# Kernel tuning notes

Measured on AMD Instinct MI355X. Metric: run time of the kernel, lower is better.

The kernel has to match this reference:

```python
import jax, jax.numpy as jnp
import numpy as np

NBITS = 4
GROUP_SIZE = 128


def setup_inputs() -> dict:
    key = jax.random.key(0)
    k1, k2, k3, k4, k5 = jax.random.split(key, 5)
    B, S, K, N = 2, 2048, 4096, 4096
    G = K // GROUP_SIZE  # 32 groups along K
    x = jax.random.normal(k1, (B, S, K), dtype=jnp.float16)
    # unpacked uint4 weights stored in int32 carrier, values in [0, 2^nbits)
    W_q = jax.random.randint(k2, (N, K), 0, 2 ** NBITS, dtype=jnp.int32)
    scale = (jax.random.uniform(k3, (N, G), dtype=jnp.float32) * 0.01 + 0.001).astype(jnp.float16)
    zero = (jax.random.uniform(k4, (N, G), dtype=jnp.float32) * (2 ** NBITS)).astype(jnp.float16)
    bias = jax.random.normal(k5, (N,), dtype=jnp.float16)
    return {"x": x, "W_q": W_q, "scale": scale, "zero": zero, "bias": bias}


def _dequant(W_q, scale, zero):
    # W_q: [N, K] int, scale/zero: [N, K//group_size] fp16
    # zeros_mode='original': W = (W_q - zero) * scale, per group along K
    N, K = W_q.shape
    G = K // GROUP_SIZE
    Wg = W_q.reshape(N, G, GROUP_SIZE).astype(jnp.float16)
    Wd = (Wg - zero[:, :, None]) * scale[:, :, None]
    return Wd.reshape(N, K)


def reference(x, W_q, scale, zero, bias):
    # out = x @ W_deq^T + bias   (layout 'nt': W is [N, K])
    W = _dequant(W_q, scale, zero)            # [N, K] fp16
    out = jnp.einsum('bsk,nk->bsn', x, W)     # [B, S, N] fp16 accum per module config
    return out + bias
```

## Files before the change

kernel.cpp:

```cpp
#include <hip/hip_runtime.h>
#include <hip/hip_bf16.h>


typedef __bf16 bf16x8 __attribute__((ext_vector_type(8)));
typedef float f32x4 __attribute__((ext_vector_type(4)));

#define BM 128
#define BN 128
#define BK 64

static __device__ __forceinline__ int pack_bf16x2(float a, float b) {
    __hip_bfloat162 p = __float22bfloat162_rn(make_float2(a, b));
    int r;
    __builtin_memcpy(&r, &p, 4);
    return r;
}

__global__ __launch_bounds__(256) void prepass_kernel(
    const float* __restrict__ X, unsigned short* __restrict__ Ad,
    const int*   __restrict__ Wq,
    const float* __restrict__ scale,
    const float* __restrict__ zero,
    unsigned short* __restrict__ Wd,
    int aUnits, int wUnits, int K, int G, int GROUP)
{
    const int stride = gridDim.x * blockDim.x;
    const int t0     = blockIdx.x * blockDim.x + threadIdx.x;

    for (int u = t0; u < aUnits; u += stride) {
        const long long f = (long long)u * 8;
        const float4 a0 = *(const float4*)(X + f);
        const float4 a1 = *(const float4*)(X + f + 4);
        int4 d;
        d.x = pack_bf16x2(a0.x, a0.y);
        d.y = pack_bf16x2(a0.z, a0.w);
        d.z = pack_bf16x2(a1.x, a1.y);
        d.w = pack_bf16x2(a1.z, a1.w);
        *(int4*)(Ad + f) = d;
    }

    const int unitsPerRow = K >> 3;
    for (int u = t0; u < wUnits; u += stride) {
        const int n = u / unitsPerRow;
        const int k = (u - n * unitsPerRow) * 8;
        const int g = k / GROUP;
        const float s  = scale[(long long)n * G + g];
        const float z  = zero [(long long)n * G + g];
        const float mz = -z * s;

        const long long f = (long long)n * K + k;
        const int4 q0 = *(const int4*)(Wq + f);
        const int4 q1 = *(const int4*)(Wq + f + 4);
        int4 d;
        d.x = pack_bf16x2((float)q0.x * s + mz, (float)q0.y * s + mz);
        d.y = pack_bf16x2((float)q0.z * s + mz, (float)q0.w * s + mz);
        d.z = pack_bf16x2((float)q1.x * s + mz, (float)q1.y * s + mz);
        d.w = pack_bf16x2((float)q1.z * s + mz, (float)q1.w * s + mz);
        *(int4*)(Wd + f) = d;
    }
}

__global__ __launch_bounds__(512, 2) void gemm256_8ph(
    const unsigned short* __restrict__ A,
    const unsigned short* __restrict__ Bw,
    const float* __restrict__ bias,
    float*       __restrict__ C,
    int M, int N, int K)
{
    __shared__ unsigned short ldsA[2][2][8192];
    __shared__ unsigned short ldsB[2][2][8192];

    const int tid  = threadIdx.x;
    const int lane = tid & 63;
    const int wave = tid >> 6;
    const int wm   = wave >> 2;
    const int wn   = wave & 3;

    const int nwg  = (N >> 8) * (M >> 8);
    const int cpx  = nwg >> 3;
    const int bid  = blockIdx.x;
    const int wgid = (bid & 7) * cpx + (bid >> 3);
    const int bx   = wgid % (N >> 8);
    const int by   = wgid / (N >> 8);
    const int blockN0 = bx << 8;
    const int blockM0 = by << 8;

    long long gSrcA[2], gSrcB[2];
    int ldsDst[2];
#pragma unroll
    for (int l = 0; l < 2; ++l) {
        const int s  = l * 512 + tid;
        const int R  = s >> 3;
        const int j  = s & 7;
        const int ju = j ^ (R & 7);
        const int r  = 2 * R + (ju >> 2);
        const int cc = ju & 3;
        gSrcA[l] = (long long)(blockM0 + r) * K + cc * 8;
        gSrcB[l] = (long long)(blockN0 + r) * K + cc * 8;
        ldsDst[l] = (l * 512 + wave * 64) * 8;
    }

    const int row16 = lane & 15;
    const int quad  = lane >> 4;
    int offA[8], offB[4];
#pragma unroll
    for (int m = 0; m < 8; ++m) {
        const int r = wm * 128 + m * 16 + row16;
        const int R = r >> 1;
        const int j = (((r & 1) << 2) | quad) ^ (R & 7);
        offA[m] = R * 64 + j * 8;
    }
#pragma unroll
    for (int n = 0; n < 4; ++n) {
        const int r = wn * 64 + n * 16 + row16;
        const int R = r >> 1;
        const int j = (((r & 1) << 2) | quad) ^ (R & 7);
        offB[n] = R * 64 + j * 8;
    }

    f32x4 acc[8][4];
#pragma unroll
    for (int m = 0; m < 8; ++m)
#pragma unroll
        for (int n = 0; n < 4; ++n)
            acc[m][n] = (f32x4){0.f, 0.f, 0.f, 0.f};

#define STAGE_A(T_, KH_)                                                      \
    do {                                                                      \
        const int b_ = (T_) & 1;                                              \
        const long long ko_ = (long long)(T_) * 64 + (KH_) * 32;              \
        __builtin_amdgcn_global_load_lds(                                     \
            (const __attribute__((address_space(1))) unsigned int*)           \
                (A + gSrcA[0] + ko_),                                         \
            (__attribute__((address_space(3))) unsigned int*)                 \
                (&ldsA[b_][KH_][ldsDst[0]]), 16, 0, 0);                       \
        __builtin_amdgcn_global_load_lds(                                     \
            (const __attribute__((address_space(1))) unsigned int*)           \
                (A + gSrcA[1] + ko_),                                         \
            (__attribute__((address_space(3))) unsigned int*)                 \
                (&ldsA[b_][KH_][ldsDst[1]]), 16, 0, 0);                       \
    } while (0)

#define STAGE_B(T_, KH_)                                                      \
    do {                                                                      \
        const int b_ = (T_) & 1;                                              \
        const long long ko_ = (long long)(T_) * 64 + (KH_) * 32;              \
        __builtin_amdgcn_global_load_lds(                                     \
            (const __attribute__((address_space(1))) unsigned int*)           \
                (Bw + gSrcB[0] + ko_),                                        \
            (__attribute__((address_space(3))) unsigned int*)                 \
                (&ldsB[b_][KH_][ldsDst[0]]), 16, 0, 0);                       \
        __builtin_amdgcn_global_load_lds(                                     \
            (const __attribute__((address_space(1))) unsigned int*)           \
                (Bw + gSrcB[1] + ko_),                                        \
            (__attribute__((address_space(3))) unsigned int*)                 \
                (&ldsB[b_][KH_][ldsDst[1]]), 16, 0, 0);                       \
    } while (0)

#define READ_BV(c_, kk_)                                                      \
    bv0 = *(const bf16x8*)&ldsB[c_][kk_][offB[0]];                            \
    bv1 = *(const bf16x8*)&ldsB[c_][kk_][offB[1]];                            \
    bv2 = *(const bf16x8*)&ldsB[c_][kk_][offB[2]];                            \
    bv3 = *(const bf16x8*)&ldsB[c_][kk_][offB[3]];

#define READ_AV(c_, kk_, mh_)                                                 \
    av0 = *(const bf16x8*)&ldsA[c_][kk_][offA[(mh_) * 4 + 0]];                \
    av1 = *(const bf16x8*)&ldsA[c_][kk_][offA[(mh_) * 4 + 1]];                \
    av2 = *(const bf16x8*)&ldsA[c_][kk_][offA[(mh_) * 4 + 2]];                \
    av3 = *(const bf16x8*)&ldsA[c_][kk_][offA[(mh_) * 4 + 3]];

#define MFROW(mi_, av_)                                                       \
    acc[mi_][0] = __builtin_amdgcn_mfma_f32_16x16x32_bf16(av_, bv0, acc[mi_][0], 0, 0, 0); \
    acc[mi_][1] = __builtin_amdgcn_mfma_f32_16x16x32_bf16(av_, bv1, acc[mi_][1], 0, 0, 0); \
    acc[mi_][2] = __builtin_amdgcn_mfma_f32_16x16x32_bf16(av_, bv2, acc[mi_][2], 0, 0, 0); \
    acc[mi_][3] = __builtin_amdgcn_mfma_f32_16x16x32_bf16(av_, bv3, acc[mi_][3], 0, 0, 0);

#define MFMA16(mh_)                                                           \
    __builtin_amdgcn_s_setprio(1);                                            \
    MFROW((mh_) * 4 + 0, av0);                                                \
    MFROW((mh_) * 4 + 1, av1);                                                \
    MFROW((mh_) * 4 + 2, av2);                                                \
    MFROW((mh_) * 4 + 3, av3);                                                \
    __builtin_amdgcn_s_setprio(0);

    const int NT = K >> 6;

    STAGE_A(0, 0); STAGE_B(0, 0); STAGE_A(0, 1); STAGE_B(0, 1);
    STAGE_A(1, 0); STAGE_B(1, 0); STAGE_A(1, 1);
    asm volatile("s_waitcnt vmcnt(6)" ::: "memory");
    __builtin_amdgcn_s_barrier();

    bf16x8 av0, av1, av2, av3, bv0, bv1, bv2, bv3;

#pragma unroll 2
    for (int T = 0; T <= NT - 3; ++T) {
        const int c = T & 1;
        READ_BV(c, 0);
        READ_AV(c, 0, 0);
        STAGE_B(T + 1, 1);
        __builtin_amdgcn_s_barrier();
        MFMA16(0);
        READ_AV(c, 0, 1);
        STAGE_A(T + 2, 0);
        __builtin_amdgcn_s_barrier();
        MFMA16(1);
        READ_BV(c, 1);
        READ_AV(c, 1, 0);
        STAGE_B(T + 2, 0);
        __builtin_amdgcn_s_barrier();
        MFMA16(0);
        READ_AV(c, 1, 1);
        STAGE_A(T + 2, 1);
        asm volatile("s_waitcnt vmcnt(6)" ::: "memory");
        __builtin_amdgcn_s_barrier();
        MFMA16(1);
    }

    STAGE_B(NT - 1, 1);
    asm volatile("s_waitcnt vmcnt(0)" ::: "memory");
    __builtin_amdgcn_s_barrier();
    {
        const int c = (NT - 2) & 1;
        READ_BV(c, 0); READ_AV(c, 0, 0); MFMA16(0);
        READ_AV(c, 0, 1); MFMA16(1);
        READ_BV(c, 1); READ_AV(c, 1, 0); MFMA16(0);
        READ_AV(c, 1, 1); MFMA16(1);
    }
    {
        const int c = (NT - 1) & 1;
        READ_BV(c, 0); READ_AV(c, 0, 0); MFMA16(0);
        READ_AV(c, 0, 1); MFMA16(1);
        READ_BV(c, 1); READ_AV(c, 1, 0); MFMA16(0);
        READ_AV(c, 1, 1); MFMA16(1);
    }

#undef STAGE_A
#undef STAGE_B
#undef READ_BV
#undef READ_AV
#undef MFROW
#undef MFMA16

    const int colBase = blockN0 + wn * 64;
    const int rowBase = blockM0 + wm * 128;
    float biasf[4];
#pragma unroll
    for (int n = 0; n < 4; ++n)
        biasf[n] = bias[colBase + n * 16 + row16];

#pragma unroll
    for (int m = 0; m < 8; ++m) {
        const int row0 = rowBase + m * 16 + quad * 4;
#pragma unroll
        for (int n = 0; n < 4; ++n) {
            const int col = colBase + n * 16 + row16;
#pragma unroll
            for (int r = 0; r < 4; ++r) {
                C[(long long)(row0 + r) * N + col] = acc[m][n][r] + biasf[n];
            }
        }
    }
}

__global__ __launch_bounds__(256, 2) void gemm_bf16_nt(
    const unsigned short* __restrict__ A,
    const unsigned short* __restrict__ Bw,
    const float* __restrict__ bias,
    float*       __restrict__ C,
    int M, int N, int K)
{
    __shared__ unsigned short ldsA[BM * BK];
    __shared__ unsigned short ldsB[BN * BK];

    const int tid   = threadIdx.x;
    const int lane  = tid & 63;
    const int wave  = tid >> 6;
    const int waveM = wave >> 1;
    const int waveN = wave & 1;

    const int blockN0 = blockIdx.x * BN;
    const int blockM0 = blockIdx.y * BM;

    const long long aBase = (long long)blockM0 * K;
    const long long bBase = (long long)blockN0 * K;

    const int rowInChunk = lane >> 3;
    const int colChunkSw = (lane & 7) ^ rowInChunk;
    const int col8       = colChunkSw * 8;

    f32x4 acc[4][4];
#pragma unroll
    for (int i = 0; i < 4; ++i)
#pragma unroll
        for (int j = 0; j < 4; ++j)
            acc[i][j] = (f32x4){0.f, 0.f, 0.f, 0.f};

    const int row16 = lane & 15;
    const int quad  = lane >> 4;
    const int sw    = row16 & 7;

    for (int k0 = 0; k0 < K; k0 += BK) {
        __syncthreads();
#pragma unroll
        for (int c = 0; c < 4; ++c) {
            const int chunk = (wave << 2) | c;
            const int row   = (chunk << 3) | rowInChunk;
            const unsigned short* gA = A  + aBase + (long long)row * K + k0 + col8;
            const unsigned short* gB = Bw + bBase + (long long)row * K + k0 + col8;
            __builtin_amdgcn_global_load_lds(
                (const __attribute__((address_space(1))) unsigned int*)gA,
                (__attribute__((address_space(3))) unsigned int*)&ldsA[chunk * 512],
                16, 0, 0);
            __builtin_amdgcn_global_load_lds(
                (const __attribute__((address_space(1))) unsigned int*)gB,
                (__attribute__((address_space(3))) unsigned int*)&ldsB[chunk * 512],
                16, 0, 0);
        }
        __syncthreads();

#pragma unroll
        for (int kk = 0; kk < 2; ++kk) {
            bf16x8 av[4], bv[4];
#pragma unroll
            for (int i = 0; i < 4; ++i) {
                const int r    = waveM * 64 + i * 16 + row16;
                const int slot = (kk * 4 + quad) ^ sw;
                av[i] = *(const bf16x8*)&ldsA[r * BK + slot * 8];
            }
#pragma unroll
            for (int j = 0; j < 4; ++j) {
                const int r    = waveN * 64 + j * 16 + row16;
                const int slot = (kk * 4 + quad) ^ sw;
                bv[j] = *(const bf16x8*)&ldsB[r * BK + slot * 8];
            }
#pragma unroll
            for (int i = 0; i < 4; ++i)
#pragma unroll
                for (int j = 0; j < 4; ++j)
                    acc[i][j] = __builtin_amdgcn_mfma_f32_16x16x32_bf16(
                        av[i], bv[j], acc[i][j], 0, 0, 0);
        }
    }

    const int colBase = blockN0 + waveN * 64;
    const int rowBase = blockM0 + waveM * 64;
    float biasf[4];
#pragma unroll
    for (int j = 0; j < 4; ++j)
        biasf[j] = bias[colBase + j * 16 + row16];

#pragma unroll
    for (int i = 0; i < 4; ++i) {
        const int row0 = rowBase + i * 16 + quad * 4;
#pragma unroll
        for (int j = 0; j < 4; ++j) {
            const int col = colBase + j * 16 + row16;
#pragma unroll
            for (int r = 0; r < 4; ++r) {
                C[(long long)(row0 + r) * N + col] = acc[i][j][r] + biasf[j];
            }
        }
    }
}

__global__ __launch_bounds__(256) void hqq_gemm_fused_f32(
    const float* __restrict__ A,
    const int*   __restrict__ Wq,
    const float* __restrict__ scale,
    const float* __restrict__ zero,
    const float* __restrict__ bias,
    float*       __restrict__ C,
    int M, int N, int K, int G, int GROUP)
{
    __shared__ unsigned short ldsA[BM * BK];
    __shared__ unsigned short ldsB[BN * BK];

    const int tid   = threadIdx.x;
    const int lane  = tid & 63;
    const int wave  = tid >> 6;
    const int waveM = wave >> 1;
    const int waveN = wave & 1;

    const int blockN0 = blockIdx.x * BN;
    const int blockM0 = blockIdx.y * BM;

    const int row16 = lane & 15;
    const int quad  = lane >> 4;

    f32x4 acc[4][4];
#pragma unroll
    for (int i = 0; i < 4; ++i)
#pragma unroll
        for (int j = 0; j < 4; ++j)
            acc[i][j] = (f32x4){0.f, 0.f, 0.f, 0.f};

    for (int k0 = 0; k0 < K; k0 += BK) {
        const int g = k0 / GROUP;
        int4 ra[4], rb[4];
#pragma unroll
        for (int c = 0; c < 4; ++c) {
            const int chunk = c * 256 + tid;
            const int row   = chunk >> 3;
            const int col   = (chunk & 7) * 8;

            const float* ap = A + (long long)(blockM0 + row) * K + k0 + col;
            const float4 a0 = *(const float4*)(ap);
            const float4 a1 = *(const float4*)(ap + 4);
            int4 da;
            da.x = pack_bf16x2(a0.x, a0.y);
            da.y = pack_bf16x2(a0.z, a0.w);
            da.z = pack_bf16x2(a1.x, a1.y);
            da.w = pack_bf16x2(a1.z, a1.w);
            ra[c] = da;

            const int n = blockN0 + row;
            const float s  = scale[(long long)n * G + g];
            const float z  = zero [(long long)n * G + g];
            const float mz = -z * s;
            const long long wb = (long long)n * K + k0 + col;
            const int4 q0 = *(const int4*)(Wq + wb);
            const int4 q1 = *(const int4*)(Wq + wb + 4);
            int4 db;
            db.x = pack_bf16x2((float)q0.x * s + mz, (float)q0.y * s + mz);
            db.y = pack_bf16x2((float)q0.z * s + mz, (float)q0.w * s + mz);
            db.z = pack_bf16x2((float)q1.x * s + mz, (float)q1.y * s + mz);
            db.w = pack_bf16x2((float)q1.z * s + mz, (float)q1.w * s + mz);
            rb[c] = db;
        }

        __syncthreads();
#pragma unroll
        for (int c = 0; c < 4; ++c) {
            const int chunk = c * 256 + tid;
            *(int4*)&ldsA[chunk * 8] = ra[c];
            *(int4*)&ldsB[chunk * 8] = rb[c];
        }
        __syncthreads();

#pragma unroll
        for (int kk = 0; kk < 2; ++kk) {
            const int kOff = kk * 32 + quad * 8;
            bf16x8 av[4], bv[4];
#pragma unroll
            for (int i = 0; i < 4; ++i)
                av[i] = *(const bf16x8*)&ldsA[(waveM * 64 + i * 16 + row16) * BK + kOff];
#pragma unroll
            for (int j = 0; j < 4; ++j)
                bv[j] = *(const bf16x8*)&ldsB[(waveN * 64 + j * 16 + row16) * BK + kOff];
#pragma unroll
            for (int i = 0; i < 4; ++i)
#pragma unroll
                for (int j = 0; j < 4; ++j)
                    acc[i][j] = __builtin_amdgcn_mfma_f32_16x16x32_bf16(
                        av[i], bv[j], acc[i][j], 0, 0, 0);
        }
    }

    const int colBase = blockN0 + waveN * 64;
    const int rowBase = blockM0 + waveM * 64;
    float biasf[4];
#pragma unroll
    for (int j = 0; j < 4; ++j)
        biasf[j] = bias[colBase + j * 16 + row16];

#pragma unroll
    for (int i = 0; i < 4; ++i) {
        const int row0 = rowBase + i * 16 + quad * 4;
#pragma unroll
        for (int j = 0; j < 4; ++j) {
            const int col = colBase + j * 16 + row16;
#pragma unroll
            for (int r = 0; r < 4; ++r) {
                C[(long long)(row0 + r) * N + col] = acc[i][j][r] + biasf[j];
            }
        }
    }
}

extern "C" void kernel_launch(void* const* d_in, const int* in_sizes, int n_in,
                              void* d_out, int out_size, void* d_ws, size_t ws_size,
                              hipStream_t stream) {
    (void)n_in; (void)out_size;

    const float* x     = (const float*)d_in[0];
    const int*   Wq    = (const int*)d_in[1];
    const float* scale = (const float*)d_in[2];
    const float* zero  = (const float*)d_in[3];
    const float* bias  = (const float*)d_in[4];
    float*       out   = (float*)d_out;

    const int N     = in_sizes[4];
    const int G     = in_sizes[2] / N;
    const int K     = in_sizes[1] / N;
    const int M     = in_sizes[0] / K;
    const int GROUP = K / G;

    const size_t needWs = (size_t)N * K * 2 + (size_t)M * K * 2;

    if (ws_size >= needWs) {
        unsigned short* Wd = (unsigned short*)d_ws;
        unsigned short* Ad = (unsigned short*)((char*)d_ws + (size_t)N * K * 2);

        const int aUnits = (int)((long long)M * K / 8);
        const int wUnits = (int)((long long)N * K / 8);
        prepass_kernel<<<2048, 256, 0, stream>>>(x, Ad, Wq, scale, zero, Wd,
                                                 aUnits, wUnits, K, G, GROUP);

        const int nwg = (N >> 8) * (M >> 8);
        const int NT  = K >> 6;
        if ((M % 256) == 0 && (N % 256) == 0 && (K % 64) == 0 && NT >= 4 &&
            (nwg % 8) == 0) {
            gemm256_8ph<<<nwg, 512, 0, stream>>>(Ad, Wd, bias, out, M, N, K);
        } else {
            dim3 grid(N / BN, M / BM);
            gemm_bf16_nt<<<grid, 256, 0, stream>>>(Ad, Wd, bias, out, M, N, K);
        }
    } else {
        dim3 grid(N / BN, M / BM);
        hqq_gemm_fused_f32<<<grid, 256, 0, stream>>>(x, Wq, scale, zero, bias, out,
                                                     M, N, K, G, GROUP);
    }
}
```

Before: 283.9 us.

## Fuse dequant and bf16 conversion into pipelined 256x256 GEMM, drop prepass

Removes the separate prepass that converted x to bf16 and dequantized W into workspace. The 256x256 GEMM now loads fp32 activations and int32 weights into registers, converts and dequantizes them, and writes bf16 into LDS inside a restructured software pipeline with explicit vmcnt waits. This avoids writing and re-reading the bf16 copies through memory. In exchange each tile moves twice as many global bytes (fp32/int32 instead of bf16), uses more VGPRs, and gives up the direct global-to-LDS load path.

```diff
diff --git a/kernel.cpp b/kernel.cpp
--- a/kernel.cpp
+++ b/kernel.cpp
@@ -4,10 +4,6 @@
 
 typedef __bf16 bf16x8 __attribute__((ext_vector_type(8)));
 typedef float f32x4 __attribute__((ext_vector_type(4)));
-
-#define BM 128
-#define BN 128
-#define BK 64
 
 static __device__ __forceinline__ int pack_bf16x2(float a, float b) {
     __hip_bfloat162 p = __float22bfloat162_rn(make_float2(a, b));
@@ -16,56 +12,17 @@
     return r;
 }
 
-__global__ __launch_bounds__(256) void prepass_kernel(
-    const float* __restrict__ X, unsigned short* __restrict__ Ad,
+struct ARegs { float4 v[2][2]; };
+struct BRegs { int4   q[2][2]; };
+
+__global__ __launch_bounds__(512, 2) void hqq_gemm256_fused(
+    const float* __restrict__ X,
     const int*   __restrict__ Wq,
     const float* __restrict__ scale,
     const float* __restrict__ zero,
-    unsigned short* __restrict__ Wd,
-    int aUnits, int wUnits, int K, int G, int GROUP)
-{
-    const int stride = gridDim.x * blockDim.x;
-    const int t0     = blockIdx.x * blockDim.x + threadIdx.x;
-
-    for (int u = t0; u < aUnits; u += stride) {
-        const long long f = (long long)u * 8;
-        const float4 a0 = *(const float4*)(X + f);
-        const float4 a1 = *(const float4*)(X + f + 4);
-        int4 d;
-        d.x = pack_bf16x2(a0.x, a0.y);
-        d.y = pack_bf16x2(a0.z, a0.w);
-        d.z = pack_bf16x2(a1.x, a1.y);
-        d.w = pack_bf16x2(a1.z, a1.w);
-        *(int4*)(Ad + f) = d;
-    }
-
-    const int unitsPerRow = K >> 3;
-    for (int u = t0; u < wUnits; u += stride) {
-        const int n = u / unitsPerRow;
-        const int k = (u - n * unitsPerRow) * 8;
-        const int g = k / GROUP;
-        const float s  = scale[(long long)n * G + g];
-        const float z  = zero [(long long)n * G + g];
-        const float mz = -z * s;
-
-        const long long f = (long long)n * K + k;
-        const int4 q0 = *(const int4*)(Wq + f);
-        const int4 q1 = *(const int4*)(Wq + f + 4);
-        int4 d;
-        d.x = pack_bf16x2((float)q0.x * s + mz, (float)q0.y * s + mz);
-        d.y = pack_bf16x2((float)q0.z * s + mz, (float)q0.w * s + mz);
-        d.z = pack_bf16x2((float)q1.x * s + mz, (float)q1.y * s + mz);
-        d.w = pack_bf16x2((float)q1.z * s + mz, (float)q1.w * s + mz);
-        *(int4*)(Wd + f) = d;
-    }
-}
-
-__global__ __launch_bounds__(512, 2) void gemm256_8ph(
-    const unsigned short* __restrict__ A,
-    const unsigned short* __restrict__ Bw,
     const float* __restrict__ bias,
     float*       __restrict__ C,
-    int M, int N, int K)
+    int M, int N, int K, int G)
 {
     __shared__ unsigned short ldsA[2][2][8192];
     __shared__ unsigned short ldsB[2][2][8192];
@@ -86,7 +43,7 @@
     const int blockM0 = by << 8;
 
     long long gSrcA[2], gSrcB[2];
-    int ldsDst[2];
+    int nIdx[2], wrElem[2];
 #pragma unroll
     for (int l = 0; l < 2; ++l) {
         const int s  = l * 512 + tid;
@@ -95,9 +52,10 @@
         const int ju = j ^ (R & 7);
         const int r  = 2 * R + (ju >> 2);
         const int cc = ju & 3;
-        gSrcA[l] = (long long)(blockM0 + r) * K + cc * 8;
-        gSrcB[l] = (long long)(blockN0 + r) * K + cc * 8;
-        ldsDst[l] = (l * 512 + wave * 64) * 8;
+        gSrcA[l]  = (long long)(blockM0 + r) * K + cc * 8;
+        gSrcB[l]  = (long long)(blockN0 + r) * K + cc * 8;
+        nIdx[l]   = blockN0 + r;
+        wrElem[l] = s * 8;
     }
 
     const int row16 = lane & 15;
@@ -125,36 +83,63 @@
         for (int n = 0; n < 4; ++n)
             acc[m][n] = (f32x4){0.f, 0.f, 0.f, 0.f};
 
-#define STAGE_A(T_, KH_)                                                      \
+#define LOAD_A(dst_, T_, KH_)                                                 \
     do {                                                                      \
-        const int b_ = (T_) & 1;                                              \
         const long long ko_ = (long long)(T_) * 64 + (KH_) * 32;              \
-        __builtin_amdgcn_global_load_lds(                                     \
-            (const __attribute__((address_space(1))) unsigned int*)           \
-                (A + gSrcA[0] + ko_),                                         \
-            (__attribute__((address_space(3))) unsigned int*)                 \
-                (&ldsA[b_][KH_][ldsDst[0]]), 16, 0, 0);                       \
-        __builtin_amdgcn_global_load_lds(                                     \
-            (const __attribute__((address_space(1))) unsigned int*)           \
-                (A + gSrcA[1] + ko_),                                         \
-            (__attribute__((address_space(3))) unsigned int*)                 \
-                (&ldsA[b_][KH_][ldsDst[1]]), 16, 0, 0);                       \
+        _Pragma("unroll")                                                     \
+        for (int l = 0; l < 2; ++l) {                                         \
+            const float* p_ = X + gSrcA[l] + ko_;                             \
+            dst_.v[l][0] = *(const float4*)p_;                                \
+            dst_.v[l][1] = *(const float4*)(p_ + 4);                          \
+        }                                                                     \
     } while (0)
 
-#define STAGE_B(T_, KH_)                                                      \
+#define LOAD_B(dst_, T_, KH_)                                                 \
     do {                                                                      \
-        const int b_ = (T_) & 1;                                              \
         const long long ko_ = (long long)(T_) * 64 + (KH_) * 32;              \
-        __builtin_amdgcn_global_load_lds(                                     \
-            (const __attribute__((address_space(1))) unsigned int*)           \
-                (Bw + gSrcB[0] + ko_),                                        \
-            (__attribute__((address_space(3))) unsigned int*)                 \
-                (&ldsB[b_][KH_][ldsDst[0]]), 16, 0, 0);                       \
-        __builtin_amdgcn_global_load_lds(                                     \
-            (const __attribute__((address_space(1))) unsigned int*)           \
-                (Bw + gSrcB[1] + ko_),                                        \
-            (__attribute__((address_space(3))) unsigned int*)                 \
-                (&ldsB[b_][KH_][ldsDst[1]]), 16, 0, 0);                       \
+        _Pragma("unroll")                                                     \
+        for (int l = 0; l < 2; ++l) {                                         \
+            const int* p_ = Wq + gSrcB[l] + ko_;                              \
+            dst_.q[l][0] = *(const int4*)p_;                                  \
+            dst_.q[l][1] = *(const int4*)(p_ + 4);                           \
+        }                                                                     \
+    } while (0)
+
+#define WRITE_A(buf_, kh_, rgs_)                                              \
+    do {                                                                      \
+        _Pragma("unroll")                                                     \
+        for (int l = 0; l < 2; ++l) {                                         \
+            int4 d_;                                                          \
+            d_.x = pack_bf16x2(rgs_.v[l][0].x, rgs_.v[l][0].y);               \
+            d_.y = pack_bf16x2(rgs_.v[l][0].z, rgs_.v[l][0].w);               \
+            d_.z = pack_bf16x2(rgs_.v[l][1].x, rgs_.v[l][1].y);               \
+            d_.w = pack_bf16x2(rgs_.v[l][1].z, rgs_.v[l][1].w);               \
+            *(int4*)&ldsA[buf_][kh_][wrElem[l]] = d_;                         \
+        }                                                                     \
+    } while (0)
+
+#define WRITE_B(buf_, kh_, rgs_, s0_, z0_, s1_, z1_)                          \
+    do {                                                                      \
+        {                                                                     \
+            const float s_ = (s0_), mz_ = -(z0_) * (s0_);                     \
+            const int4 q0_ = rgs_.q[0][0], q1_ = rgs_.q[0][1];                \
+            int4 d_;                                                          \
+            d_.x = pack_bf16x2((float)q0_.x * s_ + mz_, (float)q0_.y * s_ + mz_); \
+            d_.y = pack_bf16x2((float)q0_.z * s_ + mz_, (float)q0_.w * s_ + mz_); \
+            d_.z = pack_bf16x2((float)q1_.x * s_ + mz_, (float)q1_.y * s_ + mz_); \
+            d_.w = pack_bf16x2((float)q1_.z * s_ + mz_, (float)q1_.w * s_ + mz_); \
+            *(int4*)&ldsB[buf_][kh_][wrElem[0]] = d_;                         \
+        }                                                                     \
+        {                                                                     \
+            const float s_ = (s1_), mz_ = -(z1_) * (s1_);                     \
+            const int4 q0_ = rgs_.q[1][0], q1_ = rgs_.q[1][1];                \
+            int4 d_;                                                          \
+            d_.x = pack_bf16x2((float)q0_.x * s_ + mz_, (float)q0_.y * s_ + mz_); \
+            d_.y = pack_bf16x2((float)q0_.z * s_ + mz_, (float)q0_.w * s_ + mz_); \
+            d_.z = pack_bf16x2((float)q1_.x * s_ + mz_, (float)q1_.y * s_ + mz_); \
+            d_.w = pack_bf16x2((float)q1_.z * s_ + mz_, (float)q1_.w * s_ + mz_); \
+            *(int4*)&ldsB[buf_][kh_][wrElem[1]] = d_;                         \
+        }                                                                     \
     } while (0)
 
 #define READ_BV(c_, kk_)                                                      \
@@ -183,63 +168,116 @@
     MFROW((mh_) * 4 + 3, av3);                                                \
     __builtin_amdgcn_s_setprio(0);
 
+#define VMW(n_)  asm volatile("s_waitcnt vmcnt(" #n_ ")" ::: "memory")
+#define LGKM0()  asm volatile("s_waitcnt lgkmcnt(0)" ::: "memory")
+#define BAR()    __builtin_amdgcn_s_barrier()
+
     const int NT = K >> 6;
 
-    STAGE_A(0, 0); STAGE_B(0, 0); STAGE_A(0, 1); STAGE_B(0, 1);
-    STAGE_A(1, 0); STAGE_B(1, 0); STAGE_A(1, 1);
-    asm volatile("s_waitcnt vmcnt(6)" ::: "memory");
-    __builtin_amdgcn_s_barrier();
+    ARegs a00, a01, a10, A_f1;
+    BRegs b00, b01, b11, B_i0;
+    float sP0, sP1, zP0, zP1;
+    sP0 = scale[(long long)nIdx[0] * G];
+    sP1 = scale[(long long)nIdx[1] * G];
+    zP0 = zero [(long long)nIdx[0] * G];
+    zP1 = zero [(long long)nIdx[1] * G];
+    LOAD_A(a00, 0, 0); LOAD_B(b00, 0, 0);
+    LOAD_A(a01, 0, 1); LOAD_B(b01, 0, 1);
+    LOAD_A(a10, 1, 0); LOAD_B(b11, 1, 1);
+    VMW(0);
+    WRITE_A(0, 0, a00); WRITE_B(0, 0, b00, sP0, zP0, sP1, zP1);
+    WRITE_A(0, 1, a01); WRITE_B(0, 1, b01, sP0, zP0, sP1, zP1);
+    WRITE_A(1, 0, a10); WRITE_B(1, 1, b11, sP0, zP0, sP1, zP1);
+    LOAD_A(A_f1, 1, 1);
+    LOAD_B(B_i0, 1, 0);
+    LGKM0(); BAR();
 
     bf16x8 av0, av1, av2, av3, bv0, bv1, bv2, bv3;
 
 #pragma unroll 2
     for (int T = 0; T <= NT - 3; ++T) {
-        const int c = T & 1;
+        const int c = T & 1, cn = c ^ 1;
+        ARegs A_f0n, A_f1n;
+        BRegs B_i1n, B_i0n;
+        float sN0, sN1, zN0, zN1;
         READ_BV(c, 0);
         READ_AV(c, 0, 0);
-        STAGE_B(T + 1, 1);
-        __builtin_amdgcn_s_barrier();
+        VMW(4);
+        WRITE_A(cn, 1, A_f1);
+        {
+            const long long g2 = (T + 2) >> 1;
+            sN0 = scale[(long long)nIdx[0] * G + g2];
+            zN0 = zero [(long long)nIdx[0] * G + g2];
+            sN1 = scale[(long long)nIdx[1] * G + g2];
+            zN1 = zero [(long long)nIdx[1] * G + g2];
+        }
+        LOAD_A(A_f0n, T + 2, 0);
+        LGKM0(); BAR();
         MFMA16(0);
         READ_AV(c, 0, 1);
-        STAGE_A(T + 2, 0);
-        __builtin_amdgcn_s_barrier();
+        VMW(8);
+        WRITE_B(cn, 0, B_i0, sP0, zP0, sP1, zP1);
+        LOAD_B(B_i1n, T + 2, 1);
+        LGKM0(); BAR();
         MFMA16(1);
         READ_BV(c, 1);
         READ_AV(c, 1, 0);
-        STAGE_B(T + 2, 0);
-        __builtin_amdgcn_s_barrier();
+        VMW(4);
+        WRITE_A(c, 0, A_f0n);
+        LOAD_A(A_f1n, T + 2, 1);
+        LGKM0(); BAR();
         MFMA16(0);
         READ_AV(c, 1, 1);
-        STAGE_A(T + 2, 1);
-        asm volatile("s_waitcnt vmcnt(6)" ::: "memory");
-        __builtin_amdgcn_s_barrier();
-        MFMA16(1);
-    }
-
-    STAGE_B(NT - 1, 1);
-    asm volatile("s_waitcnt vmcnt(0)" ::: "memory");
-    __builtin_amdgcn_s_barrier();
+        VMW(4);
+        WRITE_B(c, 1, B_i1n, sN0, zN0, sN1, zN1);
+        LOAD_B(B_i0n, T + 2, 0);
+        LGKM0(); BAR();
+        MFMA16(1);
+        A_f1 = A_f1n; B_i0 = B_i0n;
+        sP0 = sN0; sP1 = sN1; zP0 = zN0; zP1 = zN1;
+    }
+
     {
-        const int c = (NT - 2) & 1;
-        READ_BV(c, 0); READ_AV(c, 0, 0); MFMA16(0);
-        READ_AV(c, 0, 1); MFMA16(1);
-        READ_BV(c, 1); READ_AV(c, 1, 0); MFMA16(0);
-        READ_AV(c, 1, 1); MFMA16(1);
-    }
-    {
-        const int c = (NT - 1) & 1;
-        READ_BV(c, 0); READ_AV(c, 0, 0); MFMA16(0);
-        READ_AV(c, 0, 1); MFMA16(1);
-        READ_BV(c, 1); READ_AV(c, 1, 0); MFMA16(0);
-        READ_AV(c, 1, 1); MFMA16(1);
-    }
-
-#undef STAGE_A
-#undef STAGE_B
+        const int c2 = (NT - 2) & 1, c1 = (NT - 1) & 1;
+        READ_BV(c2, 0);
+        READ_AV(c2, 0, 0);
+        VMW(4);
+        WRITE_A(c1, 1, A_f1);
+        LGKM0(); BAR();
+        MFMA16(0);
+        READ_AV(c2, 0, 1);
+        VMW(0);
+        WRITE_B(c1, 0, B_i0, sP0, zP0, sP1, zP1);
+        LGKM0(); BAR();
+        MFMA16(1);
+        READ_BV(c2, 1);
+        READ_AV(c2, 1, 0);
+        MFMA16(0);
+        READ_AV(c2, 1, 1);
+        MFMA16(1);
+        READ_BV(c1, 0);
+        READ_AV(c1, 0, 0);
+        MFMA16(0);
+        READ_AV(c1, 0, 1);
+        MFMA16(1);
+        READ_BV(c1, 1);
+        READ_AV(c1, 1, 0);
+        MFMA16(0);
+        READ_AV(c1, 1, 1);
+        MFMA16(1);
+    }
+
+#undef LOAD_A
+#undef LOAD_B
+#undef WRITE_A
+#undef WRITE_B
 #undef READ_BV
 #undef READ_AV
 #undef MFROW
 #undef MFMA16
+#undef VMW
+#undef LGKM0
+#undef BAR
 
     const int colBase = blockN0 + wn * 64;
     const int rowBase = blockM0 + wm * 128;
@@ -262,106 +300,9 @@
     }
 }
 
-__global__ __launch_bounds__(256, 2) void gemm_bf16_nt(
-    const unsigned short* __restrict__ A,
-    const unsigned short* __restrict__ Bw,
-    const float* __restrict__ bias,
-    float*       __restrict__ C,
-    int M, int N, int K)
-{
-    __shared__ unsigned short ldsA[BM * BK];
-    __shared__ unsigned short ldsB[BN * BK];
-
-    const int tid   = threadIdx.x;
-    const int lane  = tid & 63;
-    const int wave  = tid >> 6;
-    const int waveM = wave >> 1;
-    const int waveN = wave & 1;
-
-    const int blockN0 = blockIdx.x * BN;
-    const int blockM0 = blockIdx.y * BM;
-
-    const long long aBase = (long long)blockM0 * K;
-    const long long bBase = (long long)blockN0 * K;
-
-    const int rowInChunk = lane >> 3;
-    const int colChunkSw = (lane & 7) ^ rowInChunk;
-    const int col8       = colChunkSw * 8;
-
-    f32x4 acc[4][4];
-#pragma unroll
-    for (int i = 0; i < 4; ++i)
-#pragma unroll
-        for (int j = 0; j < 4; ++j)
-            acc[i][j] = (f32x4){0.f, 0.f, 0.f, 0.f};
-
-    const int row16 = lane & 15;
-    const int quad  = lane >> 4;
-    const int sw    = row16 & 7;
-
-    for (int k0 = 0; k0 < K; k0 += BK) {
-        __syncthreads();
-#pragma unroll
-        for (int c = 0; c < 4; ++c) {
-            const int chunk = (wave << 2) | c;
-            const int row   = (chunk << 3) | rowInChunk;
-            const unsigned short* gA = A  + aBase + (long long)row * K + k0 + col8;
-            const unsigned short* gB = Bw + bBase + (long long)row * K + k0 + col8;
-            __builtin_amdgcn_global_load_lds(
-                (const __attribute__((address_space(1))) unsigned int*)gA,
-                (__attribute__((address_space(3))) unsigned int*)&ldsA[chunk * 512],
-                16, 0, 0);
-            __builtin_amdgcn_global_load_lds(
-                (const __attribute__((address_space(1))) unsigned int*)gB,
-                (__attribute__((address_space(3))) unsigned int*)&ldsB[chunk * 512],
-                16, 0, 0);
-        }
-        __syncthreads();
-
-#pragma unroll
-        for (int kk = 0; kk < 2; ++kk) {
-            bf16x8 av[4], bv[4];
-#pragma unroll
-            for (int i = 0; i < 4; ++i) {
-                const int r    = waveM * 64 + i * 16 + row16;
-                const int slot = (kk * 4 + quad) ^ sw;
-                av[i] = *(const bf16x8*)&ldsA[r * BK + slot * 8];
-            }
-#pragma unroll
-            for (int j = 0; j < 4; ++j) {
-                const int r    = waveN * 64 + j * 16 + row16;
-                const int slot = (kk * 4 + quad) ^ sw;
-                bv[j] = *(const bf16x8*)&ldsB[r * BK + slot * 8];
-            }
-#pragma unroll
-            for (int i = 0; i < 4; ++i)
-#pragma unroll
-                for (int j = 0; j < 4; ++j)
-                    acc[i][j] = __builtin_amdgcn_mfma_f32_16x16x32_bf16(
-                        av[i], bv[j], acc[i][j], 0, 0, 0);
-        }
-    }
-
-    const int colBase = blockN0 + waveN * 64;
-    const int rowBase = blockM0 + waveM * 64;
-    float biasf[4];
-#pragma unroll
-    for (int j = 0; j < 4; ++j)
-        biasf[j] = bias[colBase + j * 16 + row16];
-
-#pragma unroll
-    for (int i = 0; i < 4; ++i) {
-        const int row0 = rowBase + i * 16 + quad * 4;
-#pragma unroll
-        for (int j = 0; j < 4; ++j) {
-            const int col = colBase + j * 16 + row16;
-#pragma unroll
-            for (int r = 0; r < 4; ++r) {
-                C[(long long)(row0 + r) * N + col] = acc[i][j][r] + biasf[j];
-            }
-        }
-    }
-}
+#define BM 128
+#define BN 128
+#define BK 64
 
 __global__ __launch_bounds__(256) void hqq_gemm_fused_f32(
     const float* __restrict__ A,
@@ -480,7 +421,7 @@
 extern "C" void kernel_launch(void* const* d_in, const int* in_sizes, int n_in,
                               void* d_out, int out_size, void* d_ws, size_t ws_size,
                               hipStream_t stream) {
-    (void)n_in; (void)out_size;
+    (void)n_in; (void)out_size; (void)d_ws; (void)ws_size;
 
     const float* x     = (const float*)d_in[0];
     const int*   Wq    = (const int*)d_in[1];
@@ -495,26 +436,12 @@
     const int M     = in_sizes[0] / K;
     const int GROUP = K / G;
 
-    const size_t needWs = (size_t)N * K * 2 + (size_t)M * K * 2;
-
-    if (ws_size >= needWs) {
-        unsigned short* Wd = (unsigned short*)d_ws;
-        unsigned short* Ad = (unsigned short*)((char*)d_ws + (size_t)N * K * 2);
-
-        const int aUnits = (int)((long long)M * K / 8);
-        const int wUnits = (int)((long long)N * K / 8);
-        prepass_kernel<<<2048, 256, 0, stream>>>(x, Ad, Wq, scale, zero, Wd,
-                                                 aUnits, wUnits, K, G, GROUP);
-
-        const int nwg = (N >> 8) * (M >> 8);
-        const int NT  = K >> 6;
-        if ((M % 256) == 0 && (N % 256) == 0 && (K % 64) == 0 && NT >= 4 &&
-            (nwg % 8) == 0) {
-            gemm256_8ph<<<nwg, 512, 0, stream>>>(Ad, Wd, bias, out, M, N, K);
-        } else {
-            dim3 grid(N / BN, M / BM);
-            gemm_bf16_nt<<<grid, 256, 0, stream>>>(Ad, Wd, bias, out, M, N, K);
-        }
+    const int nwg = (N >> 8) * (M >> 8);
+    const int NT  = K >> 6;
+    if ((M % 256) == 0 && (N % 256) == 0 && (K % 64) == 0 && NT >= 4 &&
+        (nwg % 8) == 0 && GROUP == 128) {
+        hqq_gemm256_fused<<<nwg, 512, 0, stream>>>(x, Wq, scale, zero, bias, out,
+                                                   M, N, K, G);
     } else {
         dim3 grid(N / BN, M / BM);
         hqq_gemm_fused_f32<<<grid, 256, 0, stream>>>(x, Wq, scale, zero, bias, out,
```

Result: slower. 416.0 us (+46.5%).
